# Performance work log

Hardware: AMD Instinct MI355X
Metric: run time of the kernel (lower is better)

The kernel has to match this reference:

```python
import jax, jax.numpy as jnp
import numpy as np

B, T, E = 8, 2048, 1024  # batch, seq_len, emb_size (= output_emb_size)


def setup_inputs() -> dict:
    key = jax.random.key(0)
    k1, k2, k3, k4, k5, k6, k7 = jax.random.split(key, 7)
    return {
        "q": jax.random.normal(k1, (B, T, E), jnp.float32),
        "k": jax.random.normal(k2, (B, T, E), jnp.float32),
        "v": jax.random.normal(k3, (B, T, E), jnp.float32),
        "mask": jax.random.randint(k4, (T, T), 0, 2, jnp.int32),
        # nn.Linear weights, stored [out, in] as in torch; applied as x @ W.T
        "Wq": jax.random.normal(k5, (E, E), jnp.float32) / np.sqrt(E),
        "Wk": jax.random.normal(k6, (E, E), jnp.float32) / np.sqrt(E),
        "Wv": jax.random.normal(k7, (E, E), jnp.float32) / np.sqrt(E),
    }


def reference(q, k, v, mask, Wq, Wk, Wv):
    # QKV projections (bias-free Linear): x @ W.T
    query = jnp.einsum("bte,oe->bto", q, Wq)
    key_p = jnp.einsum("bse,oe->bso", k, Wk)
    value = jnp.einsum("bse,oe->bso", v, Wv)
    d = key_p.shape[-1]
    scores = jnp.einsum("bto,bso->bts", query, key_p) / np.sqrt(d).astype(jnp.float32)
    # torch.any(mask): mask is nonzero somewhere -> apply masked_fill(mask==0, -inf)
    scores = jnp.where(mask[None, :, :] == 0, -jnp.inf, scores)
    weights = jax.nn.softmax(scores, axis=-1)
    return jnp.einsum("bts,bso->bto", weights, value)
```

## Files before the change

### kernel.cpp

```cpp
#include <hip/hip_runtime.h>
#include <hip/hip_bf16.h>

typedef __attribute__((ext_vector_type(8))) short short8;
typedef __attribute__((ext_vector_type(8))) unsigned short ushortx8;
typedef __attribute__((ext_vector_type(4))) unsigned short ushortx4;
typedef __attribute__((ext_vector_type(4))) float floatx4;

#define NB 8
#define NT 2048
#define NE 1024

__device__ __forceinline__ unsigned short f2bf(float f){
  unsigned int u = __builtin_bit_cast(unsigned int, f);
  u += 0x7FFFu + ((u >> 16) & 1u);
  return (unsigned short)(u >> 16);
}
__device__ __forceinline__ float bf2f(unsigned short h){
  unsigned int u = ((unsigned int)h) << 16;
  return __builtin_bit_cast(float, u);
}

__device__ __forceinline__ void async16(void* lds, const void* g){
  __builtin_amdgcn_global_load_lds(
      (const __attribute__((address_space(1))) unsigned int*)g,
      (__attribute__((address_space(3))) unsigned int*)lds, 16, 0, 0);
}

__global__ __launch_bounds__(256) void cvt3(const float* __restrict__ a0,
                                            const float* __restrict__ a1,
                                            const float* __restrict__ a2,
                                            unsigned short* __restrict__ out,
                                            int n4_per){
  const float* src = blockIdx.y == 0 ? a0 : (blockIdx.y == 1 ? a1 : a2);
  unsigned short* dst = out + (size_t)blockIdx.y * (size_t)n4_per * 4;
  int i = blockIdx.x * 256 + threadIdx.x;
  if (i < n4_per){
    floatx4 f = ((const floatx4*)src)[i];
    ushortx4 o;
    o.x = f2bf(f.x); o.y = f2bf(f.y); o.z = f2bf(f.z); o.w = f2bf(f.w);
    *(ushortx4*)(dst + (size_t)i * 4) = o;
  }
}

__global__ __launch_bounds__(256) void pack_mask(const int* __restrict__ m,
                                                 unsigned long long* __restrict__ bits){
  int t = blockIdx.x * 256 + threadIdx.x;
  const int4* p = (const int4*)(m + (size_t)t * 64);
  unsigned long long w = 0;
  #pragma unroll
  for (int jj = 0; jj < 16; jj++){
    int4 v = p[jj];
    w |= (unsigned long long)(v.x != 0) << (jj * 4 + 0);
    w |= (unsigned long long)(v.y != 0) << (jj * 4 + 1);
    w |= (unsigned long long)(v.z != 0) << (jj * 4 + 2);
    w |= (unsigned long long)(v.w != 0) << (jj * 4 + 3);
  }
  bits[t] = w;
}

template<int EPI>
__global__ __launch_bounds__(512, 2) void gemm_nt(
    const unsigned short* __restrict__ A, long strideA,
    const unsigned short* __restrict__ B, long strideB,
    void* __restrict__ Out, long strideOutBytes,
    const unsigned long long* __restrict__ mbits,
    int K, int gx, int gy)
{
  __shared__ __attribute__((aligned(16))) unsigned short As[3 * 256 * 64];
  __shared__ __attribute__((aligned(16))) unsigned short Bs[3 * 128 * 64];
  const int tid = threadIdx.x;
  const int lane = tid & 63, wave = tid >> 6;

  int L = blockIdx.x;
  int xcd = L & 7, tt = L >> 3;
  int x = tt % gx;
  int strip = xcd + ((tt / gx) << 3);
  int y = strip % gy, z = strip / gy;
  const int m0 = y << 8, n0 = x << 7;
  const int Nn = gx << 7;

  const unsigned short* Az = A + (size_t)z * strideA;
  const unsigned short* Bz = B + (size_t)z * strideB;

  const char* gA[4]; int loA[4];
  #pragma unroll
  for (int i = 0; i < 4; i++){
    int s = (wave << 8) + (i << 6) + lane;
    int row = s >> 3, c = (s & 7) ^ (row & 7);
    loA[i] = s << 4;
    gA[i] = (const char*)(Az + (size_t)(m0 + row) * K) + (c << 4);
  }
  const char* gB[2]; int loB[2];
  #pragma unroll
  for (int i = 0; i < 2; i++){
    int s = (wave << 7) + (i << 6) + lane;
    int row = s >> 3, c = (s & 7) ^ (row & 7);
    loB[i] = s << 4;
    gB[i] = (const char*)(Bz + (size_t)(n0 + row) * K) + (c << 4);
  }
  char* AsB = (char*)As;
  char* BsB = (char*)Bs;

  const int lm = lane & 15, qd = lane >> 4;
  const int wr = (wave >> 1) << 6, wc = (wave & 1) << 6;
  const int sw = lm & 7;
  const int offA0 = (wr + lm) * 128 + ((qd ^ sw) << 4);
  const int offA1 = (wr + lm) * 128 + (((4 + qd) ^ sw) << 4);
  const int offB0 = (wc + lm) * 128 + ((qd ^ sw) << 4);
  const int offB1 = (wc + lm) * 128 + (((4 + qd) ^ sw) << 4);

  floatx4 acc[4][4];
  floatx4 zero4 = {0.f, 0.f, 0.f, 0.f};
  #pragma unroll
  for (int a = 0; a < 4; a++)
    #pragma unroll
    for (int b = 0; b < 4; b++) acc[a][b] = zero4;

  auto stage = [&](int buf){
    char* Ad = AsB + (buf << 15);
    char* Bd = BsB + (buf << 14);
    #pragma unroll
    for (int i = 0; i < 4; i++){ async16(Ad + loA[i], gA[i]); gA[i] += 128; }
    #pragma unroll
    for (int i = 0; i < 2; i++){ async16(Bd + loB[i], gB[i]); gB[i] += 128; }
  };

  auto compute = [&](int b){
    const char* ab = AsB + (b << 15);
    const char* bb = BsB + (b << 14);
    short8 a0[4], a1[4], b0[4], b1[4];
    #pragma unroll
    for (int mi = 0; mi < 4; mi++) a0[mi] = *(const short8*)(ab + offA0 + mi * 2048);
    #pragma unroll
    for (int ni = 0; ni < 4; ni++) b0[ni] = *(const short8*)(bb + offB0 + ni * 2048);
    __builtin_amdgcn_s_setprio(1);
    #pragma unroll
    for (int mi = 0; mi < 4; mi++)
      #pragma unroll
      for (int ni = 0; ni < 4; ni++)
        acc[mi][ni] = __builtin_amdgcn_mfma_f32_16x16x32_bf16(a0[mi], b0[ni], acc[mi][ni], 0, 0, 0);
    __builtin_amdgcn_s_setprio(0);
    #pragma unroll
    for (int mi = 0; mi < 4; mi++) a1[mi] = *(const short8*)(ab + offA1 + mi * 2048);
    #pragma unroll
    for (int ni = 0; ni < 4; ni++) b1[ni] = *(const short8*)(bb + offB1 + ni * 2048);
    __builtin_amdgcn_s_setprio(1);
    #pragma unroll
    for (int mi = 0; mi < 4; mi++)
      #pragma unroll
      for (int ni = 0; ni < 4; ni++)
        acc[mi][ni] = __builtin_amdgcn_mfma_f32_16x16x32_bf16(a1[mi], b1[ni], acc[mi][ni], 0, 0, 0);
    __builtin_amdgcn_s_setprio(0);
  };

  const int NK = K >> 6;
  stage(0);
  stage(1);
  asm volatile("s_waitcnt vmcnt(6)\n\ts_barrier" ::: "memory");

  int b = 0, bs = 2;
  for (int t = 0; t < NK - 2; ++t){
    stage(bs);
    compute(b);
    asm volatile("s_waitcnt vmcnt(6)\n\ts_barrier" ::: "memory");
    b  = (b  == 2) ? 0 : b  + 1;
    bs = (bs == 2) ? 0 : bs + 1;
  }
  compute(b);
  asm volatile("s_waitcnt vmcnt(0)\n\ts_barrier" ::: "memory");
  b = (b == 2) ? 0 : b + 1;
  compute(b);

  char* OutZ = (char*)Out + (size_t)z * strideOutBytes;
  if constexpr (EPI == 1){
    int wcol = (n0 + wc) >> 6;
    #pragma unroll
    for (int mi = 0; mi < 4; mi++){
      #pragma unroll
      for (int i = 0; i < 4; i++){
        int row = m0 + wr + mi * 16 + qd * 4 + i;
        unsigned long long w = mbits[(size_t)row * (NT / 64) + wcol];
        unsigned short* po = (unsigned short*)OutZ + (size_t)row * Nn + n0 + wc;
        #pragma unroll
        for (int ni = 0; ni < 4; ni++){
          float vv = acc[mi][ni][i];
          float s = ((w >> (ni * 16 + lm)) & 1ull) ? vv * 0.03125f : -INFINITY;
          po[ni * 16 + lm] = f2bf(s);
        }
      }
    }
  } else {
    #pragma unroll
    for (int mi = 0; mi < 4; mi++){
      #pragma unroll
      for (int i = 0; i < 4; i++){
        int row = m0 + wr + mi * 16 + qd * 4 + i;
        #pragma unroll
        for (int ni = 0; ni < 4; ni++){
          int col = n0 + wc + ni * 16 + lm;
          float vv = acc[mi][ni][i];
          if constexpr (EPI == 0)
            ((unsigned short*)OutZ)[(size_t)row * Nn + col] = f2bf(vv);
          else
            ((float*)OutZ)[(size_t)row * Nn + col] = vv;
        }
      }
    }
  }
}

__global__ __launch_bounds__(256) void transpose_bf16(const unsigned short* __restrict__ in,
                                                      unsigned short* __restrict__ out,
                                                      int rows, int cols){
  __shared__ __attribute__((aligned(16))) unsigned short tile[64][72];
  const unsigned short* ib = in + (size_t)blockIdx.z * rows * cols;
  unsigned short* ob = out + (size_t)blockIdx.z * rows * cols;
  int r0 = blockIdx.x * 64;
  int c0 = blockIdx.y * 64;
  int tid = threadIdx.x;
  #pragma unroll
  for (int i = 0; i < 2; i++){
    int id = tid + i * 256;
    int r = id >> 3, c = (id & 7) * 8;
    ushortx8 v = *(const ushortx8*)(ib + (size_t)(r0 + r) * cols + c0 + c);
    *(ushortx8*)&tile[r][c] = v;
  }
  __syncthreads();
  #pragma unroll
  for (int i = 0; i < 2; i++){
    int id = tid + i * 256;
    int r = id >> 3, c = (id & 7) * 8;
    ushortx8 v;
    #pragma unroll
    for (int j = 0; j < 8; j++) v[j] = tile[c + j][r];
    *(ushortx8*)(ob + (size_t)(c0 + r) * rows + r0 + c) = v;
  }
}

__global__ __launch_bounds__(256) void softmax_rows(unsigned short* __restrict__ S){
  size_t row = blockIdx.x;
  unsigned short* p = S + row * NT;
  int tid = threadIdx.x;
  ushortx8 v = *(const ushortx8*)(p + tid * 8);
  float f[8];
  #pragma unroll
  for (int j = 0; j < 8; j++) f[j] = bf2f(v[j]);
  float mx = f[0];
  #pragma unroll
  for (int j = 1; j < 8; j++) mx = fmaxf(mx, f[j]);
  #pragma unroll
  for (int off = 32; off > 0; off >>= 1) mx = fmaxf(mx, __shfl_xor(mx, off, 64));
  __shared__ float redm[4], reds[4];
  int lane = tid & 63, wv = tid >> 6;
  if (lane == 0) redm[wv] = mx;
  __syncthreads();
  mx = fmaxf(fmaxf(redm[0], redm[1]), fmaxf(redm[2], redm[3]));
  float e[8]; float se = 0.f;
  #pragma unroll
  for (int j = 0; j < 8; j++){ e[j] = __expf(f[j] - mx); se += e[j]; }
  #pragma unroll
  for (int off = 32; off > 0; off >>= 1) se += __shfl_xor(se, off, 64);
  if (lane == 0) reds[wv] = se;
  __syncthreads();
  se = reds[0] + reds[1] + reds[2] + reds[3];
  float inv = 1.f / se;
  ushortx8 o;
  #pragma unroll
  for (int j = 0; j < 8; j++) o[j] = f2bf(e[j] * inv);
  *(ushortx8*)(p + tid * 8) = o;
}

extern "C" void kernel_launch(void* const* d_in, const int* in_sizes, int n_in,
                              void* d_out, int out_size, void* d_ws, size_t ws_size,
                              hipStream_t stream){
  const float* q  = (const float*)d_in[0];
  const float* k  = (const float*)d_in[1];
  const float* v  = (const float*)d_in[2];
  const int* mask = (const int*)d_in[3];
  const float* Wq = (const float*)d_in[4];
  const float* Wk = (const float*)d_in[5];
  const float* Wv = (const float*)d_in[6];

  const size_t BTE = (size_t)NB * NT * NE;
  unsigned short* ws   = (unsigned short*)d_ws;
  unsigned short* QKVp = ws;
  unsigned short* VpT  = ws + 3 * BTE;
  unsigned short* Sb   = ws + 3 * BTE + BTE;
  unsigned short* Qin  = ws + 3 * BTE;
  unsigned short* Wb   = ws + 3 * BTE + BTE + (size_t)NB * NT * NT;
  unsigned long long* mbits = (unsigned long long*)(Wb + (size_t)3 * NE * NE);

  unsigned short* Qp = QKVp;
  unsigned short* Kp = QKVp + BTE;
  unsigned short* Vp = QKVp + 2 * BTE;

  cvt3<<<dim3(16384, 3), 256, 0, stream>>>(q, k, v, Qin, (int)(BTE / 4));
  cvt3<<<dim3(1024, 3), 256, 0, stream>>>(Wq, Wk, Wv, Wb, NE * NE / 4);
  pack_mask<<<256, 256, 0, stream>>>(mask, mbits);

  gemm_nt<0><<<1536, 512, 0, stream>>>(
      Qin, (long)BTE, Wb, (long)NE * NE,
      QKVp, (long)BTE * 2, nullptr, NE, 8, 64);

  transpose_bf16<<<dim3(32, 16, 8), 256, 0, stream>>>(Vp, VpT, NT, NE);

  gemm_nt<1><<<1024, 512, 0, stream>>>(
      Qp, (long)NT * NE, Kp, (long)NT * NE,
      Sb, (long)NT * NT * 2, mbits, NE, 16, 8);

  softmax_rows<<<dim3(NB * NT), 256, 0, stream>>>(Sb);

  gemm_nt<2><<<512, 512, 0, stream>>>(
      Sb, (long)NT * NT, VpT, (long)NE * NT,
      d_out, (long)NT * NE * 4, nullptr, NT, 8, 8);
}
```

Baseline: 586.3 us.

## Enlarge GEMM tiles to 256x256 with a split-half double-buffered LDS pipeline

Reworks the shared bf16 NT GEMM from 256x128 tiles with a 3-stage buffer to 256x256 tiles. It uses a 128KB LDS double buffer whose K-step is split into two 32-wide halves, and staging of the next tile is interleaved between four MFMA phases. Each wave now computes a 128x64 sub-tile with 32 accumulators, which raises MFMA work per LDS fragment load and halves the grid for all three GEMMs. The costs are much higher register and LDS use (likely one block per CU), more barriers per K iteration, and fewer blocks to fill the machine.

```diff
diff --git a/kernel.cpp b/kernel.cpp
--- a/kernel.cpp
+++ b/kernel.cpp
@@ -25,6 +25,9 @@
       (const __attribute__((address_space(1))) unsigned int*)g,
       (__attribute__((address_space(3))) unsigned int*)lds, 16, 0, 0);
 }
+
+#define MFMA16(d, va, vb) \
+  d = __builtin_amdgcn_mfma_f32_16x16x32_bf16(va, vb, d, 0, 0, 0)
 
 __global__ __launch_bounds__(256) void cvt3(const float* __restrict__ a0,
                                             const float* __restrict__ a1,
@@ -66,8 +69,7 @@
     const unsigned long long* __restrict__ mbits,
     int K, int gx, int gy)
 {
-  __shared__ __attribute__((aligned(16))) unsigned short As[3 * 256 * 64];
-  __shared__ __attribute__((aligned(16))) unsigned short Bs[3 * 128 * 64];
+  __shared__ __attribute__((aligned(16))) char Lds[131072];
   const int tid = threadIdx.x;
   const int lane = tid & 63, wave = tid >> 6;
 
@@ -76,111 +78,124 @@
   int x = tt % gx;
   int strip = xcd + ((tt / gx) << 3);
   int y = strip % gy, z = strip / gy;
-  const int m0 = y << 8, n0 = x << 7;
-  const int Nn = gx << 7;
+  const int m0 = y << 8, n0 = x << 8;
+  const int Nn = gx << 8;
 
   const unsigned short* Az = A + (size_t)z * strideA;
   const unsigned short* Bz = B + (size_t)z * strideB;
 
-  const char* gA[4]; int loA[4];
-  #pragma unroll
-  for (int i = 0; i < 4; i++){
-    int s = (wave << 8) + (i << 6) + lane;
-    int row = s >> 3, c = (s & 7) ^ (row & 7);
-    loA[i] = s << 4;
-    gA[i] = (const char*)(Az + (size_t)(m0 + row) * K) + (c << 4);
-  }
-  const char* gB[2]; int loB[2];
-  #pragma unroll
-  for (int i = 0; i < 2; i++){
-    int s = (wave << 7) + (i << 6) + lane;
-    int row = s >> 3, c = (s & 7) ^ (row & 7);
-    loB[i] = s << 4;
-    gB[i] = (const char*)(Bz + (size_t)(n0 + row) * K) + (c << 4);
-  }
-  char* AsB = (char*)As;
-  char* BsB = (char*)Bs;
+  const long rowb  = (long)K * 2;
+  const long rs128 = rowb << 7;
+  const int r0 = tid >> 2;
+  const int c0 = (tid & 3) ^ (r0 & 3);
+  const char* pA0 = (const char*)Az + (size_t)(m0 + r0) * rowb + (c0 << 4);
+  const char* pA1 = pA0 + 64;
+  const char* pB0 = (const char*)Bz + (size_t)(n0 + r0) * rowb + (c0 << 4);
+  const char* pB1 = pB0 + 64;
+  const int stg = tid << 4;
+
+  auto stageU = [&](const char*& g, int ldsoff){
+    async16(Lds + ldsoff + stg,        g);
+    async16(Lds + ldsoff + stg + 8192, g + rs128);
+    g += 128;
+  };
 
   const int lm = lane & 15, qd = lane >> 4;
-  const int wr = (wave >> 1) << 6, wc = (wave & 1) << 6;
-  const int sw = lm & 7;
-  const int offA0 = (wr + lm) * 128 + ((qd ^ sw) << 4);
-  const int offA1 = (wr + lm) * 128 + (((4 + qd) ^ sw) << 4);
-  const int offB0 = (wc + lm) * 128 + ((qd ^ sw) << 4);
-  const int offB1 = (wc + lm) * 128 + (((4 + qd) ^ sw) << 4);
-
-  floatx4 acc[4][4];
+  const int wm = wave >> 2, wn = wave & 3;
+  const int fsw  = (qd ^ (lm & 3)) << 4;
+  const int aoff = ((wm << 7) + lm) * 64 + fsw;
+  const int boff = 32768 + ((wn << 6) + lm) * 64 + fsw;
+
+  floatx4 acc[8][4];
   floatx4 zero4 = {0.f, 0.f, 0.f, 0.f};
   #pragma unroll
-  for (int a = 0; a < 4; a++)
+  for (int a = 0; a < 8; a++)
     #pragma unroll
     for (int b = 0; b < 4; b++) acc[a][b] = zero4;
 
-  auto stage = [&](int buf){
-    char* Ad = AsB + (buf << 15);
-    char* Bd = BsB + (buf << 14);
-    #pragma unroll
-    for (int i = 0; i < 4; i++){ async16(Ad + loA[i], gA[i]); gA[i] += 128; }
-    #pragma unroll
-    for (int i = 0; i < 2; i++){ async16(Bd + loB[i], gB[i]); gB[i] += 128; }
-  };
-
-  auto compute = [&](int b){
-    const char* ab = AsB + (b << 15);
-    const char* bb = BsB + (b << 14);
-    short8 a0[4], a1[4], b0[4], b1[4];
-    #pragma unroll
-    for (int mi = 0; mi < 4; mi++) a0[mi] = *(const short8*)(ab + offA0 + mi * 2048);
-    #pragma unroll
-    for (int ni = 0; ni < 4; ni++) b0[ni] = *(const short8*)(bb + offB0 + ni * 2048);
+  const int NK = K >> 6;
+
+  stageU(pB0, 32768);
+  stageU(pA0, 0);
+  stageU(pB1, 32768 + 16384);
+  stageU(pA1, 16384);
+  stageU(pB0, 65536 + 32768);
+  stageU(pA0, 65536);
+  stageU(pB1, 65536 + 32768 + 16384);
+  asm volatile("s_waitcnt vmcnt(6)\n\ts_barrier" ::: "memory");
+
+  short8 a[4], b[4];
+  for (int t = 0; t < NK; ++t){
+    const int rb = (t & 1) << 16;
+    const int sb = rb ^ 65536;
+
+    if (t + 1 < NK) stageU(pA1, sb + 16384);
+    #pragma unroll
+    for (int j = 0; j < 4; j++) a[j] = *(const short8*)(Lds + rb + aoff + j * 1024);
+    #pragma unroll
+    for (int n = 0; n < 4; n++) b[n] = *(const short8*)(Lds + rb + boff + n * 1024);
+    asm volatile("s_waitcnt lgkmcnt(0)\n\ts_barrier" ::: "memory");
+    __builtin_amdgcn_sched_barrier(0);
     __builtin_amdgcn_s_setprio(1);
     #pragma unroll
-    for (int mi = 0; mi < 4; mi++)
-      #pragma unroll
-      for (int ni = 0; ni < 4; ni++)
-        acc[mi][ni] = __builtin_amdgcn_mfma_f32_16x16x32_bf16(a0[mi], b0[ni], acc[mi][ni], 0, 0, 0);
+    for (int j = 0; j < 4; j++)
+      #pragma unroll
+      for (int n = 0; n < 4; n++) MFMA16(acc[j][n], a[j], b[n]);
     __builtin_amdgcn_s_setprio(0);
-    #pragma unroll
-    for (int mi = 0; mi < 4; mi++) a1[mi] = *(const short8*)(ab + offA1 + mi * 2048);
-    #pragma unroll
-    for (int ni = 0; ni < 4; ni++) b1[ni] = *(const short8*)(bb + offB1 + ni * 2048);
+
+    if (t + 2 < NK) stageU(pB0, rb + 32768);
+    #pragma unroll
+    for (int j = 0; j < 4; j++) a[j] = *(const short8*)(Lds + rb + aoff + (4 + j) * 1024);
+    asm volatile("s_waitcnt lgkmcnt(0)\n\ts_barrier" ::: "memory");
+    __builtin_amdgcn_sched_barrier(0);
     __builtin_amdgcn_s_setprio(1);
     #pragma unroll
-    for (int mi = 0; mi < 4; mi++)
-      #pragma unroll
-      for (int ni = 0; ni < 4; ni++)
-        acc[mi][ni] = __builtin_amdgcn_mfma_f32_16x16x32_bf16(a1[mi], b1[ni], acc[mi][ni], 0, 0, 0);
+    for (int j = 0; j < 4; j++)
+      #pragma unroll
+      for (int n = 0; n < 4; n++) MFMA16(acc[4 + j][n], a[j], b[n]);
     __builtin_amdgcn_s_setprio(0);
-  };
-
-  const int NK = K >> 6;
-  stage(0);
-  stage(1);
-  asm volatile("s_waitcnt vmcnt(6)\n\ts_barrier" ::: "memory");
-
-  int b = 0, bs = 2;
-  for (int t = 0; t < NK - 2; ++t){
-    stage(bs);
-    compute(b);
-    asm volatile("s_waitcnt vmcnt(6)\n\ts_barrier" ::: "memory");
-    b  = (b  == 2) ? 0 : b  + 1;
-    bs = (bs == 2) ? 0 : bs + 1;
-  }
-  compute(b);
-  asm volatile("s_waitcnt vmcnt(0)\n\ts_barrier" ::: "memory");
-  b = (b == 2) ? 0 : b + 1;
-  compute(b);
+
+    if (t + 2 < NK) stageU(pA0, rb);
+    #pragma unroll
+    for (int j = 0; j < 4; j++) a[j] = *(const short8*)(Lds + rb + 16384 + aoff + j * 1024);
+    #pragma unroll
+    for (int n = 0; n < 4; n++) b[n] = *(const short8*)(Lds + rb + 16384 + boff + n * 1024);
+    asm volatile("s_waitcnt lgkmcnt(0)\n\ts_barrier" ::: "memory");
+    __builtin_amdgcn_sched_barrier(0);
+    __builtin_amdgcn_s_setprio(1);
+    #pragma unroll
+    for (int j = 0; j < 4; j++)
+      #pragma unroll
+      for (int n = 0; n < 4; n++) MFMA16(acc[j][n], a[j], b[n]);
+    __builtin_amdgcn_s_setprio(0);
+
+    if (t + 2 < NK) stageU(pB1, rb + 32768 + 16384);
+    #pragma unroll
+    for (int j = 0; j < 4; j++) a[j] = *(const short8*)(Lds + rb + 16384 + aoff + (4 + j) * 1024);
+    if (t + 2 < NK)
+      asm volatile("s_waitcnt vmcnt(6) lgkmcnt(0)\n\ts_barrier" ::: "memory");
+    else
+      asm volatile("s_waitcnt vmcnt(0) lgkmcnt(0)\n\ts_barrier" ::: "memory");
+    __builtin_amdgcn_sched_barrier(0);
+    __builtin_amdgcn_s_setprio(1);
+    #pragma unroll
+    for (int j = 0; j < 4; j++)
+      #pragma unroll
+      for (int n = 0; n < 4; n++) MFMA16(acc[4 + j][n], a[j], b[n]);
+    __builtin_amdgcn_s_setprio(0);
+  }
 
   char* OutZ = (char*)Out + (size_t)z * strideOutBytes;
+  const int colbase = n0 + (wn << 6);
   if constexpr (EPI == 1){
-    int wcol = (n0 + wc) >> 6;
-    #pragma unroll
-    for (int mi = 0; mi < 4; mi++){
+    const int wcol = colbase >> 6;
+    #pragma unroll
+    for (int mi = 0; mi < 8; mi++){
       #pragma unroll
       for (int i = 0; i < 4; i++){
-        int row = m0 + wr + mi * 16 + qd * 4 + i;
+        int row = m0 + (wm << 7) + mi * 16 + qd * 4 + i;
         unsigned long long w = mbits[(size_t)row * (NT / 64) + wcol];
-        unsigned short* po = (unsigned short*)OutZ + (size_t)row * Nn + n0 + wc;
+        unsigned short* po = (unsigned short*)OutZ + (size_t)row * Nn + colbase;
         #pragma unroll
         for (int ni = 0; ni < 4; ni++){
           float vv = acc[mi][ni][i];
@@ -191,13 +206,13 @@
     }
   } else {
     #pragma unroll
-    for (int mi = 0; mi < 4; mi++){
+    for (int mi = 0; mi < 8; mi++){
       #pragma unroll
       for (int i = 0; i < 4; i++){
-        int row = m0 + wr + mi * 16 + qd * 4 + i;
+        int row = m0 + (wm << 7) + mi * 16 + qd * 4 + i;
         #pragma unroll
         for (int ni = 0; ni < 4; ni++){
-          int col = n0 + wc + ni * 16 + lm;
+          int col = colbase + ni * 16 + lm;
           float vv = acc[mi][ni][i];
           if constexpr (EPI == 0)
             ((unsigned short*)OutZ)[(size_t)row * Nn + col] = f2bf(vv);
@@ -298,19 +313,19 @@
   cvt3<<<dim3(1024, 3), 256, 0, stream>>>(Wq, Wk, Wv, Wb, NE * NE / 4);
   pack_mask<<<256, 256, 0, stream>>>(mask, mbits);
 
-  gemm_nt<0><<<1536, 512, 0, stream>>>(
+  gemm_nt<0><<<768, 512, 0, stream>>>(
       Qin, (long)BTE, Wb, (long)NE * NE,
-      QKVp, (long)BTE * 2, nullptr, NE, 8, 64);
+      QKVp, (long)BTE * 2, nullptr, NE, 4, 64);
 
   transpose_bf16<<<dim3(32, 16, 8), 256, 0, stream>>>(Vp, VpT, NT, NE);
 
-  gemm_nt<1><<<1024, 512, 0, stream>>>(
+  gemm_nt<1><<<512, 512, 0, stream>>>(
       Qp, (long)NT * NE, Kp, (long)NT * NE,
-      Sb, (long)NT * NT * 2, mbits, NE, 16, 8);
+      Sb, (long)NT * NT * 2, mbits, NE, 8, 8);
 
   softmax_rows<<<dim3(NB * NT), 256, 0, stream>>>(Sb);
 
-  gemm_nt<2><<<512, 512, 0, stream>>>(
+  gemm_nt<2><<<256, 512, 0, stream>>>(
       Sb, (long)NT * NT, VpT, (long)NE * NT,
-      d_out, (long)NT * NE * 4, nullptr, NT, 8, 8);
-}
+      d_out, (long)NT * NE * 4, nullptr, NT, 4, 8);
+}
```

Measured after the change: 525.8 us. 1.11x faster.
